# Performance work log

Hardware: AMD Instinct MI355X
Metric: run time of the kernel (lower is better)

## Reference

```python
import jax, jax.numpy as jnp
import numpy as np

NGRAMS = (1, 2, 3, 4)


def _conv1d(x, W, b):
    # x: [B, S, E], W: [D, E, K], b: [D] -> [B, S-K+1, D] (valid conv, torch Conv1d)
    y = jax.lax.conv_general_dilated(
        x.transpose(0, 2, 1), W, window_strides=(1,), padding='VALID',
        dimension_numbers=('NCH', 'OIH', 'NCH'))
    return y.transpose(0, 2, 1) + b


def setup_inputs() -> dict:
    key = jax.random.key(0)
    ks = jax.random.split(key, 9)
    B, S, E, D = 64, 512, 256, 512
    inp = {'features': jax.random.normal(ks[0], (B, S, E), dtype=jnp.float32)}
    for i, n in enumerate(NGRAMS):
        fan_in = E * n
        inp[f'W{n}'] = jax.random.normal(ks[1 + 2 * i], (D, E, n), dtype=jnp.float32) / np.sqrt(fan_in)
        inp[f'b{n}'] = jax.random.normal(ks[2 + 2 * i], (D,), dtype=jnp.float32) * 0.01
    return inp


def reference(features, W1, b1, W2, b2, W3, b3, W4, b4):
    Ws = (W1, W2, W3, W4)
    bs = (b1, b2, b3, b4)
    # n-gram conv branches: branch g has kernel size NGRAMS[g] = g+1, length S - g
    feats = [_conv1d(features, W, b) for W, b in zip(Ws, bs)]
    B, S, E = features.shape
    flen = E  # faithful to original: features_len = features.shape[-1] (the embed dim)
    out = feats[0]  # unigram features, [B, S, D]
    i = jnp.arange(flen)
    add = jnp.zeros((B, flen, out.shape[-1]), out.dtype)
    # Original nested loops: out[:, i] += sum_{g=1}^{maxn-1} sum_{p=max(0,i-g+1)}^{min(i+1,L_g)-1} feats[g][:, p]
    # Computed here with per-branch prefix sums (exclusive) -> windowed sums.
    for g in range(1, max(NGRAMS)):
        y = feats[g]                      # [B, L, D], L = S - g
        L = y.shape[1]
        P = jnp.concatenate([jnp.zeros_like(y[:, :1]), jnp.cumsum(y, axis=1)], axis=1)  # [B, L+1, D]
        hi = jnp.minimum(i + 1, L)
        lo = jnp.minimum(jnp.maximum(0, i - g + 1), L)
        win = P[:, hi] - P[:, lo]         # [B, flen, D]
        add = add + jnp.where((hi > lo)[None, :, None], win, jnp.zeros_like(win))
    return out.at[:, :flen].add(add)
```

## Files before the change

### kernel.cpp

```cpp
#include <hip/hip_runtime.h>
#include <hip/hip_bf16.h>

#define EDIM 256
#define SDIM 512
#define BDIM 64
#define DDIM 512
#define SPAD 514

#define OFF_XP    0u
#define OFF_BFI   16842752u
#define OFF_BFT   18415616u
#define OFF_CORR  18677760u
#define OFF_BI    18939904u

#define CVT_BLOCKS  4112
#define WB_BASE     4112
#define CORR_BASE   4624
#define PREP_BLOCKS 8720

typedef __attribute__((ext_vector_type(8))) __bf16 bf16x8;
typedef __attribute__((ext_vector_type(4))) float  f32x4;
typedef __attribute__((ext_vector_type(8))) unsigned short ushort8v;

__device__ __forceinline__ unsigned short f2bf(float f) {
    unsigned int u = __float_as_uint(f);
    u = (u + 0x7fffu + ((u >> 16) & 1u)) >> 16;
    return (unsigned short)u;
}

__global__ __launch_bounds__(256) void prep_all(
    const float* __restrict__ X,
    const float* __restrict__ W1, const float* __restrict__ b1,
    const float* __restrict__ W2, const float* __restrict__ b2,
    const float* __restrict__ W3, const float* __restrict__ b3,
    const float* __restrict__ W4, const float* __restrict__ b4,
    char* __restrict__ wsb)
{
    const int tid = threadIdx.x;

    if (blockIdx.x < CVT_BLOCKS) {
        unsigned short* Xp = (unsigned short*)(wsb + OFF_XP);
        const int i   = blockIdx.x * 256 + tid;
        const int row = i >> 5;
        const int q   = i & 31;
        const int b   = row / SPAD;
        const int j   = row - b * SPAD;
        ushort8v v;
        if (j < 2) {
            v = (ushort8v)0;
        } else {
            const float* src = X + ((size_t)(b * SDIM + j - 2)) * EDIM + q * 8;
            const float4 f0 = *(const float4*)(src);
            const float4 f1 = *(const float4*)(src + 4);
            v[0] = f2bf(f0.x); v[1] = f2bf(f0.y); v[2] = f2bf(f0.z); v[3] = f2bf(f0.w);
            v[4] = f2bf(f1.x); v[5] = f2bf(f1.y); v[6] = f2bf(f1.z); v[7] = f2bf(f1.w);
        }
        *(ushort8v*)(Xp + (size_t)row * EDIM + q * 8) = v;
        return;
    }

    if (blockIdx.x < CORR_BASE) {
        const int d = blockIdx.x - WB_BASE;
        const int e = tid;
        const int de = d * EDIM + e;

        const float w1  = W1[de];
        const float w20 = W2[de * 2 + 0], w21 = W2[de * 2 + 1];
        const float w30 = W3[de * 3 + 0], w31 = W3[de * 3 + 1], w32 = W3[de * 3 + 2];
        const float w40 = W4[de * 4 + 0], w41 = W4[de * 4 + 1], w42 = W4[de * 4 + 2], w43 = W4[de * 4 + 3];

        float g[6];
        g[0] = w40;
        g[1] = w30 + w40 + w41;
        g[2] = w1 + w20 + w30 + w31 + w40 + w41 + w42;
        g[3] = w21 + w31 + w32 + w41 + w42 + w43;
        g[4] = w32 + w42 + w43;
        g[5] = w43;

        const int fm = d & 15, t = (d >> 4) & 3, h = (d >> 6) & 1, c = d >> 7;
        const int hi = (e >> 3) & 3, j = e & 7, eb = e >> 5;
        char* ibase = wsb + OFF_BFI + (size_t)((c * 2 + h) * 48) * 4096
                    + t * 1024 + hi * 256 + fm * 16 + j * 2;
#pragma unroll
        for (int s = 0; s < 6; ++s)
            *(unsigned short*)(ibase + (size_t)(s * 8 + eb) * 4096) = f2bf(g[s]);

        *(unsigned short*)(wsb + OFF_BFT + (size_t)((c * 2 + h) * 8 + eb) * 4096
                           + t * 1024 + hi * 256 + fm * 16 + j * 2) = f2bf(w1);

        if (e == 0)
            ((float*)(wsb + OFF_BI))[d] = b1[d] + b2[d] + 2.0f * b3[d] + 3.0f * b4[d];
        return;
    }

    {
        __shared__ float cls[16];
        const int cb = blockIdx.x - CORR_BASE;
        const int d  = cb >> 3;
        const int bq = (cb & 7) * 8;
        const int e  = tid;

        if (tid < 16) cls[tid] = 0.f;

        const float w31 = W3[(size_t)d * 768 + 3 * e + 1];
        const float w32 = W3[(size_t)d * 768 + 3 * e + 2];
        const float4 w4v = *(const float4*)(W4 + (size_t)d * 1024 + 4 * e);
        const float w41 = w4v.y, w42 = w4v.z, w43 = w4v.w;

        const float c00 = w31 + w41 + w42;
        const float c01 = w32 + w42 + w43;
        const float c02 = w43;
        __syncthreads();

#pragma unroll
        for (int bi = 0; bi < 8; ++bi) {
            const float* xr = X + (size_t)(bq + bi) * (SDIM * EDIM) + e;
            const float x0 = xr[0], x1 = xr[EDIM], x2 = xr[2 * EDIM];
            float a0 = c00 * x0 + c01 * x1 + c02 * x2;
            float a1 = w41 * x0 + w42 * x1 + w43 * x2;
#pragma unroll
            for (int off = 32; off >= 1; off >>= 1) {
                a0 += __shfl_xor(a0, off, 64);
                a1 += __shfl_xor(a1, off, 64);
            }
            if ((tid & 63) == 0) {
                atomicAdd(&cls[bi * 2 + 0], a0);
                atomicAdd(&cls[bi * 2 + 1], a1);
            }
        }
        __syncthreads();

        if (tid < 16) {
            const int s = tid & 1;
            const float bc = s ? b4[d] : (b3[d] + 2.f * b4[d]);
            ((float*)(wsb + OFF_CORR))[(size_t)d * 128 + bq * 2 + tid] = -cls[tid] - bc;
        }
    }
}

#define GLL(src, dst) \
    __builtin_amdgcn_global_load_lds((const __attribute__((address_space(1))) void*)(src), \
                                     (__attribute__((address_space(3))) void*)(dst), 16, 0, 0)

__global__ __launch_bounds__(512, 4) void mega(
    const unsigned short* __restrict__ Xp,
    const char* __restrict__ wsb,
    const float* __restrict__ b1,
    float* __restrict__ out)
{
    __shared__ __align__(16) char smem[32768];
    const int id  = blockIdx.x;
    const int strip = id & 127;
    const int c     = id >> 7;
    const int col0  = c * 128;
    const int tid = threadIdx.x;
    const int w = tid >> 6, l = tid & 63;

    const int sub = l >> 2;
    const int swz = (((l & 3) ^ ((sub >> 1) & 3)) * 16);
    const int ra  = strip * 128 + 16 * w + sub;
    const int ba  = ra >> 8, sa = ra & 255;

    const int oA = (16 * w) * 64;
    char* q0 = smem;
    char* q1 = smem + 8192;
    char* q2 = smem + 16384;
    char* q3 = smem + 24576;

    const int wrg = (w >> 2) * 64;
    const int qc  = w & 3;
    const int fm  = l & 15;
    const int rslot = (((l >> 4) ^ ((fm >> 1) & 3)) * 16);

    const int hq   = qc >> 1;
    const int toff = (qc & 1) * 2048;
    const char* bfi = wsb + OFF_BFI + (size_t)(c * 2 + hq) * (48 * 4096) + toff + l * 16;
    const char* bft = wsb + OFF_BFT + (size_t)(c * 2 + hq) * (8 * 4096)  + toff + l * 16;

    f32x4 acc[4][2];
    const char* ga;

    auto LOADB = [&](bf16x8 (&dst)[2], const char* base, int kt) {
#pragma unroll
        for (int j = 0; j < 2; ++j)
            dst[j] = *(const bf16x8*)(base + (size_t)kt * 4096 + j * 1024);
    };
    auto STAGE = [&](char* buf) {
        GLL(ga, buf + oA);
        ga += 64;
    };
    auto COMP = [&](const char* buf, const bf16x8 (&bfr)[2]) {
        bf16x8 af[4];
#pragma unroll
        for (int t = 0; t < 4; ++t)
            af[t] = *(const bf16x8*)(buf + (wrg + t * 16 + fm) * 64 + rslot);
#pragma unroll
        for (int i = 0; i < 4; ++i)
#pragma unroll
            for (int j = 0; j < 2; ++j)
                acc[i][j] = __builtin_amdgcn_mfma_f32_16x16x32_bf16(af[i], bfr[j], acc[i][j], 0, 0, 0);
    };

#define PHASE_W3  asm volatile("s_waitcnt vmcnt(3) lgkmcnt(0)" ::: "memory"); \
                  __builtin_amdgcn_s_barrier();
#define PHASE_W0  asm volatile("s_waitcnt vmcnt(0) lgkmcnt(0)" ::: "memory"); \
                  __builtin_amdgcn_s_barrier();
#define DO_COMP(Q, B) __builtin_amdgcn_s_setprio(1); COMP(Q, B); __builtin_amdgcn_s_setprio(0);

    auto GEMM = [&](const char* bbase, int nk) {
        bf16x8 b0[2], b1r[2], b2[2], b3[2];
        STAGE(q0); LOADB(b0,  bbase, 0);
        STAGE(q1); LOADB(b1r, bbase, 1);
#pragma unroll 1
        for (int kt = 0; kt + 4 < nk; kt += 4) {
            PHASE_W3; STAGE(q2); LOADB(b2,  bbase, kt + 2); DO_COMP(q0, b0);
            PHASE_W3; STAGE(q3); LOADB(b3,  bbase, kt + 3); DO_COMP(q1, b1r);
            PHASE_W3; STAGE(q0); LOADB(b0,  bbase, kt + 4); DO_COMP(q2, b2);
            PHASE_W3; STAGE(q1); LOADB(b1r, bbase, kt + 5); DO_COMP(q3, b3);
        }
        PHASE_W3; STAGE(q2); LOADB(b2, bbase, nk - 2); DO_COMP(q0, b0);
        PHASE_W3; STAGE(q3); LOADB(b3, bbase, nk - 1); DO_COMP(q1, b1r);
        PHASE_W3;                                      DO_COMP(q2, b2);
        PHASE_W0;                                      DO_COMP(q3, b3);
    };

    auto EPI = [&](int s_base, bool with_corr) {
        const float* bias = with_corr ? (const float*)(wsb + OFF_BI) : b1;
        const float* corr = (const float*)(wsb + OFF_CORR);
        const int ocol = col0 + qc * 32 + fm;
        const int rq   = (l >> 4) * 4;
        float bv[2];
#pragma unroll
        for (int j = 0; j < 2; ++j) bv[j] = bias[ocol + j * 16];
#pragma unroll
        for (int i = 0; i < 4; ++i) {
#pragma unroll
            for (int r = 0; r < 4; ++r) {
                const int rr  = strip * 128 + wrg + i * 16 + rq + r;
                const int ssl = rr & 255;
                const int bb  = rr >> 8;
                float* op = out + ((size_t)(bb * SDIM + s_base + ssl)) * DDIM + ocol;
                if (with_corr && ssl < 2) {
                    const float* cp = corr + (size_t)ocol * 128 + bb * 2 + ssl;
#pragma unroll
                    for (int j = 0; j < 2; ++j)
                        op[j * 16] = acc[i][j][r] + bv[j] + cp[(size_t)j * 16 * 128];
                } else {
#pragma unroll
                    for (int j = 0; j < 2; ++j)
                        op[j * 16] = acc[i][j][r] + bv[j];
                }
            }
        }
    };

#pragma unroll
    for (int i = 0; i < 4; ++i)
#pragma unroll
        for (int j = 0; j < 2; ++j) acc[i][j] = (f32x4){0.f, 0.f, 0.f, 0.f};
    ga = (const char*)(Xp + (size_t)(ba * SPAD + sa) * EDIM) + swz;
    GEMM(bfi, 48);
    EPI(0, true);

#pragma unroll
    for (int i = 0; i < 4; ++i)
#pragma unroll
        for (int j = 0; j < 2; ++j) acc[i][j] = (f32x4){0.f, 0.f, 0.f, 0.f};
    ga = (const char*)(Xp + (size_t)(ba * SPAD + 258 + sa) * EDIM) + swz;
    GEMM(bft, 8);
    EPI(256, false);
}

extern "C" void kernel_launch(void* const* d_in, const int* in_sizes, int n_in,
                              void* d_out, int out_size, void* d_ws, size_t ws_size,
                              hipStream_t stream)
{
    const float* X  = (const float*)d_in[0];
    const float* W1 = (const float*)d_in[1];
    const float* b1 = (const float*)d_in[2];
    const float* W2 = (const float*)d_in[3];
    const float* b2 = (const float*)d_in[4];
    const float* W3 = (const float*)d_in[5];
    const float* b3 = (const float*)d_in[6];
    const float* W4 = (const float*)d_in[7];
    const float* b4 = (const float*)d_in[8];
    float* out = (float*)d_out;
    char*  wsb = (char*)d_ws;

    prep_all<<<dim3(PREP_BLOCKS), dim3(256), 0, stream>>>(X, W1, b1, W2, b2, W3, b3, W4, b4, wsb);

    mega<<<dim3(512), dim3(512), 0, stream>>>(
        (const unsigned short*)(wsb + OFF_XP), wsb, b1, out);
}
```

Baseline: 159.5 us.

## Double K-step per pipeline phase with 128-byte LDS rows

Each pipeline stage now covers two K=32 slices: the A tile rows grow to 128 bytes, with two global-to-LDS loads per thread and a new XOR swizzle, and B fragments grow to four registers per stage. The number of barrier/waitcnt phases per GEMM is halved (48 to 24 and 8 to 4), which cuts synchronisation overhead and gives more MFMA work between barriers. In exchange, LDS use doubles to 64 KB per block and register pressure rises, which may reduce occupancy at 512 threads with launch bounds asking for 4 blocks per CU.

Result: no change. 158.3 us (-0.7%).

```diff
diff --git a/kernel.cpp b/kernel.cpp
--- a/kernel.cpp
+++ b/kernel.cpp
@@ -148,7 +148,7 @@
     const float* __restrict__ b1,
     float* __restrict__ out)
 {
-    __shared__ __align__(16) char smem[32768];
+    __shared__ __align__(16) char smem[65536];
     const int id  = blockIdx.x;
     const int strip = id & 127;
     const int c     = id >> 7;
@@ -156,21 +156,25 @@
     const int tid = threadIdx.x;
     const int w = tid >> 6, l = tid & 63;
 
-    const int sub = l >> 2;
-    const int swz = (((l & 3) ^ ((sub >> 1) & 3)) * 16);
-    const int ra  = strip * 128 + 16 * w + sub;
-    const int ba  = ra >> 8, sa = ra & 255;
-
-    const int oA = (16 * w) * 64;
+    const int swz = ((l & 7) ^ (l >> 3)) * 16;
+    const int r0  = strip * 128 + 16 * w + (l >> 3);
+    const int r1  = r0 + 8;
+    const int ba0 = r0 >> 8, sa0 = r0 & 255;
+    const int ba1 = r1 >> 8, sa1 = r1 & 255;
+
+    const int oA0 = (16 * w) * 128;
+    const int oA1 = oA0 + 1024;
     char* q0 = smem;
-    char* q1 = smem + 8192;
-    char* q2 = smem + 16384;
-    char* q3 = smem + 24576;
+    char* q1 = smem + 16384;
+    char* q2 = smem + 32768;
+    char* q3 = smem + 49152;
 
     const int wrg = (w >> 2) * 64;
     const int qc  = w & 3;
     const int fm  = l & 15;
-    const int rslot = (((l >> 4) ^ ((fm >> 1) & 3)) * 16);
+    const int hi4 = l >> 4;
+    const int rs0 = ((hi4)     ^ (fm & 7)) * 16;
+    const int rs1 = ((4 + hi4) ^ (fm & 7)) * 16;
 
     const int hq   = qc >> 1;
     const int toff = (qc & 1) * 2048;
@@ -178,50 +182,57 @@
     const char* bft = wsb + OFF_BFT + (size_t)(c * 2 + hq) * (8 * 4096)  + toff + l * 16;
 
     f32x4 acc[4][2];
-    const char* ga;
-
-    auto LOADB = [&](bf16x8 (&dst)[2], const char* base, int kt) {
-#pragma unroll
-        for (int j = 0; j < 2; ++j)
-            dst[j] = *(const bf16x8*)(base + (size_t)kt * 4096 + j * 1024);
+    const char *ga0, *ga1;
+
+    auto LOADB = [&](bf16x8 (&dst)[4], const char* base, int ph) {
+#pragma unroll
+        for (int ks = 0; ks < 2; ++ks)
+#pragma unroll
+            for (int j = 0; j < 2; ++j)
+                dst[ks * 2 + j] = *(const bf16x8*)(base + (size_t)(2 * ph + ks) * 4096 + j * 1024);
     };
     auto STAGE = [&](char* buf) {
-        GLL(ga, buf + oA);
-        ga += 64;
-    };
-    auto COMP = [&](const char* buf, const bf16x8 (&bfr)[2]) {
-        bf16x8 af[4];
-#pragma unroll
-        for (int t = 0; t < 4; ++t)
-            af[t] = *(const bf16x8*)(buf + (wrg + t * 16 + fm) * 64 + rslot);
-#pragma unroll
-        for (int i = 0; i < 4; ++i)
-#pragma unroll
-            for (int j = 0; j < 2; ++j)
-                acc[i][j] = __builtin_amdgcn_mfma_f32_16x16x32_bf16(af[i], bfr[j], acc[i][j], 0, 0, 0);
-    };
-
-#define PHASE_W3  asm volatile("s_waitcnt vmcnt(3) lgkmcnt(0)" ::: "memory"); \
-                  __builtin_amdgcn_s_barrier();
-#define PHASE_W0  asm volatile("s_waitcnt vmcnt(0) lgkmcnt(0)" ::: "memory"); \
-                  __builtin_amdgcn_s_barrier();
+        GLL(ga0, buf + oA0);
+        GLL(ga1, buf + oA1);
+        ga0 += 128; ga1 += 128;
+    };
+    auto COMP = [&](const char* buf, const bf16x8 (&b)[4]) {
+#pragma unroll
+        for (int ks = 0; ks < 2; ++ks) {
+            bf16x8 af[4];
+            const int rs = ks ? rs1 : rs0;
+#pragma unroll
+            for (int t = 0; t < 4; ++t)
+                af[t] = *(const bf16x8*)(buf + (wrg + t * 16 + fm) * 128 + rs);
+#pragma unroll
+            for (int i = 0; i < 4; ++i)
+#pragma unroll
+                for (int j = 0; j < 2; ++j)
+                    acc[i][j] = __builtin_amdgcn_mfma_f32_16x16x32_bf16(af[i], b[ks * 2 + j], acc[i][j], 0, 0, 0);
+        }
+    };
+
+#define PH6  asm volatile("s_waitcnt vmcnt(6) lgkmcnt(0)" ::: "memory"); \
+             __builtin_amdgcn_s_barrier();
+#define PH0  asm volatile("s_waitcnt vmcnt(0) lgkmcnt(0)" ::: "memory"); \
+             __builtin_amdgcn_s_barrier();
 #define DO_COMP(Q, B) __builtin_amdgcn_s_setprio(1); COMP(Q, B); __builtin_amdgcn_s_setprio(0);
 
-    auto GEMM = [&](const char* bbase, int nk) {
-        bf16x8 b0[2], b1r[2], b2[2], b3[2];
+    auto GEMM = [&](const char* bbase, int np) {
+        bf16x8 b0[4], b1r[4], b2[4], b3[4];
         STAGE(q0); LOADB(b0,  bbase, 0);
         STAGE(q1); LOADB(b1r, bbase, 1);
 #pragma unroll 1
-        for (int kt = 0; kt + 4 < nk; kt += 4) {
-            PHASE_W3; STAGE(q2); LOADB(b2,  bbase, kt + 2); DO_COMP(q0, b0);
-            PHASE_W3; STAGE(q3); LOADB(b3,  bbase, kt + 3); DO_COMP(q1, b1r);
-            PHASE_W3; STAGE(q0); LOADB(b0,  bbase, kt + 4); DO_COMP(q2, b2);
-            PHASE_W3; STAGE(q1); LOADB(b1r, bbase, kt + 5); DO_COMP(q3, b3);
-        }
-        PHASE_W3; STAGE(q2); LOADB(b2, bbase, nk - 2); DO_COMP(q0, b0);
-        PHASE_W3; STAGE(q3); LOADB(b3, bbase, nk - 1); DO_COMP(q1, b1r);
-        PHASE_W3;                                      DO_COMP(q2, b2);
-        PHASE_W0;                                      DO_COMP(q3, b3);
+        for (int p = 0; p + 4 < np; p += 4) {
+            PH6; STAGE(q2); LOADB(b2,  bbase, p + 2); DO_COMP(q0, b0);
+            PH6; STAGE(q3); LOADB(b3,  bbase, p + 3); DO_COMP(q1, b1r);
+            PH6; STAGE(q0); LOADB(b0,  bbase, p + 4); DO_COMP(q2, b2);
+            PH6; STAGE(q1); LOADB(b1r, bbase, p + 5); DO_COMP(q3, b3);
+        }
+        PH6; STAGE(q2); LOADB(b2, bbase, np - 2); DO_COMP(q0, b0);
+        PH6; STAGE(q3); LOADB(b3, bbase, np - 1); DO_COMP(q1, b1r);
+        PH6;                                      DO_COMP(q2, b2);
+        PH0;                                      DO_COMP(q3, b3);
     };
 
     auto EPI = [&](int s_base, bool with_corr) {
@@ -258,16 +269,18 @@
     for (int i = 0; i < 4; ++i)
 #pragma unroll
         for (int j = 0; j < 2; ++j) acc[i][j] = (f32x4){0.f, 0.f, 0.f, 0.f};
-    ga = (const char*)(Xp + (size_t)(ba * SPAD + sa) * EDIM) + swz;
-    GEMM(bfi, 48);
+    ga0 = (const char*)(Xp + (size_t)(ba0 * SPAD + sa0) * EDIM) + swz;
+    ga1 = (const char*)(Xp + (size_t)(ba1 * SPAD + sa1) * EDIM) + swz;
+    GEMM(bfi, 24);
     EPI(0, true);
 
 #pragma unroll
     for (int i = 0; i < 4; ++i)
 #pragma unroll
         for (int j = 0; j < 2; ++j) acc[i][j] = (f32x4){0.f, 0.f, 0.f, 0.f};
-    ga = (const char*)(Xp + (size_t)(ba * SPAD + 258 + sa) * EDIM) + swz;
-    GEMM(bft, 8);
+    ga0 = (const char*)(Xp + (size_t)(ba0 * SPAD + 258 + sa0) * EDIM) + swz;
+    ga1 = (const char*)(Xp + (size_t)(ba1 * SPAD + 258 + sa1) * EDIM) + swz;
+    GEMM(bft, 4);
     EPI(256, false);
 }
 
```
